# Kernel tuning notes

Hardware: AMD Instinct MI355X
Metric: run time of the kernel (lower is better)

The kernel has to match this reference:

```python
import jax, jax.numpy as jnp
import numpy as np

DIM = 1024
H = 16
HD = DIM // H
SCALE = HD ** -0.5
LAMBDA_INIT = 0.1
EPS = 1e-6


def setup_inputs() -> dict:
    key0 = jax.random.key(0)
    ks = jax.random.split(key0, 12)
    B, Nq, Nk = 2, 1024, 2048
    w = 0.02
    inp = {
        "query": jax.random.normal(ks[0], (B, Nq, DIM), jnp.float32),
        "key": jax.random.normal(ks[1], (B, Nk, DIM), jnp.float32),
        "value": jax.random.normal(ks[2], (B, Nk, DIM), jnp.float32),
        "qpos": jax.random.randint(ks[3], (B, Nq), 0, Nq, jnp.int32),
        "kpos": jax.random.randint(ks[4], (B, Nk), 0, Nk, jnp.int32),
        "q1_w": jax.random.normal(ks[5], (DIM, DIM), jnp.float32) * w,
        "q2_w": jax.random.normal(ks[6], (DIM, DIM), jnp.float32) * w,
        "kv1_w": jax.random.normal(ks[7], (2 * DIM, DIM), jnp.float32) * w,
        "kv2_w": jax.random.normal(ks[8], (2 * DIM, DIM), jnp.float32) * w,
        "proj_w": jax.random.normal(ks[9], (DIM, DIM), jnp.float32) * w,
        "proj_b": jnp.zeros((DIM,), jnp.float32),
        "norm_w": jnp.ones((DIM,), jnp.float32),
        "lambda_1": jnp.ones((1, H, 1, 1), jnp.float32),
        # layer_idx=0, max_layer=12 -> scale = 1/12
        "lambda_2": jnp.full((1, H, 1, 1), 1.0 - LAMBDA_INIT * (1.0 / 12.0), jnp.float32),
    }
    return inp


def _split_heads(x, B, N):
    # [B, N, DIM] -> [B, H, N, HD]
    return x.reshape(B, N, H, HD).transpose(0, 2, 1, 3)


def reference(query, key, value, qpos, kpos, q1_w, q2_w, kv1_w, kv2_w,
              proj_w, proj_b, norm_w, lambda_1, lambda_2):
    B, Nq, C = query.shape
    Nk = key.shape[1]

    q1 = _split_heads(query @ q1_w.T, B, Nq)
    q2 = _split_heads(query @ q2_w.T, B, Nq)

    kv1 = (key @ kv1_w.T).reshape(B, Nk, 2, H, HD).transpose(2, 0, 3, 1, 4)
    k1, v1 = kv1[0], kv1[1]  # [B, H, Nk, HD]
    kv2 = (key @ kv2_w.T).reshape(B, Nk, 2, H, HD).transpose(2, 0, 3, 1, 4)
    k2 = kv2[0]

    attn1 = jax.nn.softmax(jnp.einsum('bhqd,bhkd->bhqk', q1, k1) * SCALE, axis=-1)
    attn2 = jax.nn.softmax(jnp.einsum('bhqd,bhkd->bhqk', q2, k2) * SCALE, axis=-1)

    lambda_full = lambda_1 - lambda_2 + LAMBDA_INIT  # [1, H, 1, 1]
    diff_attn = attn1 - lambda_full * attn2

    x = jnp.einsum('bhqk,bhkd->bhqd', diff_attn, v1)
    x = x.transpose(0, 2, 1, 3).reshape(B, Nq, C)

    # RMSNorm (computed in float32 like the original)
    xf = x.astype(jnp.float32)
    xf = xf * jax.lax.rsqrt(jnp.mean(xf * xf, axis=-1, keepdims=True) + EPS) * norm_w
    x = xf.astype(x.dtype)

    return x @ proj_w.T + proj_b
```

## Files before the change

### kernel.cpp

```cpp
#include <hip/hip_runtime.h>
#include <cstdint>

typedef unsigned short u16;
typedef __bf16 bf16x8 __attribute__((ext_vector_type(8)));
typedef float f32x4 __attribute__((ext_vector_type(4)));
typedef float f32x16 __attribute__((ext_vector_type(16)));
typedef uint32_t u32x4 __attribute__((ext_vector_type(4)));

#define SCALE_LOG2E (0.125f * 1.44269504088896340736f)

__device__ __forceinline__ u16 f2bf(float f) {
    uint32_t u = __builtin_bit_cast(uint32_t, f);
    u += 0x7fff + ((u >> 16) & 1);
    return (u16)(u >> 16);
}
__device__ __forceinline__ float bf2f(u16 u) {
    return __builtin_bit_cast(float, (uint32_t)u << 16);
}

__device__ __forceinline__ void gload_lds16(const void* g, void* l) {
    __builtin_amdgcn_global_load_lds(
        (__attribute__((address_space(1))) void*)g,
        (__attribute__((address_space(3))) void*)l, 16, 0, 0);
}

__global__ __launch_bounds__(256) void cvt_all(const float* __restrict__ s0,
                                               const float* __restrict__ s1,
                                               const float* __restrict__ s2,
                                               const float* __restrict__ s3,
                                               const float* __restrict__ s4,
                                               const float* __restrict__ s5,
                                               const float* __restrict__ s6,
                                               u16* __restrict__ d0, u16* __restrict__ d1,
                                               u16* __restrict__ d2, u16* __restrict__ d3,
                                               u16* __restrict__ d4) {
    int i = blockIdx.x * 256 + threadIdx.x;
    const float* src;
    u16* dst;
    int off;
    if (i < 524288)       { src = s0; dst = d0; off = i; }
    else if (i < 1572864) { src = s1; dst = d1; off = i - 524288; }
    else if (i < 1835008) { src = s2; dst = d2; off = i - 1572864; }
    else if (i < 2097152) { src = s3; dst = d2 + (size_t)1024 * 1024; off = i - 1835008; }
    else if (i < 2621440) { src = s4; dst = d3; off = i - 2097152; }
    else if (i < 2883584) { src = s5; dst = d3 + (size_t)2048 * 1024; off = i - 2621440; }
    else                  { src = s6; dst = d4; off = i - 2883584; }
    float4 v = ((const float4*)src)[off];
    ushort4 o;
    o.x = f2bf(v.x); o.y = f2bf(v.y); o.z = f2bf(v.z); o.w = f2bf(v.w);
    ((ushort4*)dst)[off] = o;
}

__global__ __launch_bounds__(256) void gemm_qkv(const u16* __restrict__ Wq,
                                                const u16* __restrict__ Xq,
                                                const u16* __restrict__ Wkv,
                                                const u16* __restrict__ Xk,
                                                u16* __restrict__ q1s, u16* __restrict__ q2s,
                                                u16* __restrict__ k1f, u16* __restrict__ v1f,
                                                u16* __restrict__ k2f) {
    __shared__ u16 As[2][128 * 32];
    __shared__ u16 Bs[2][128 * 32];
    const int K = 1024;
    const int bid = blockIdx.x;
    int mode, bm, bn;
    const u16 *A, *B;
    if (bid < 256) {
        mode = 0; bm = bid >> 4; bn = bid & 15; A = Wq; B = Xq;
    } else {
        int t = bid - 256;
        mode = 1; bm = t % 24; bn = t / 24; A = Wkv; B = Xk;
    }
    const int tid = threadIdx.x;
    const int l = tid & 63, w = tid >> 6;
    const int c = l & 15, g = l >> 4;
    const int wr = w >> 1, wc = w & 1;

    f32x4 acc[4][4];
#pragma unroll
    for (int i = 0; i < 4; i++)
#pragma unroll
        for (int j = 0; j < 4; j++) acc[i][j] = f32x4{0.f, 0.f, 0.f, 0.f};

    const u16* Abase = A + (size_t)(bm * 128) * K;
    const u16* Bbase = B + (size_t)(bn * 128) * K;
    const int r0 = 32 * w + (l >> 2);
    const int chsw = ((l & 3) ^ ((l >> 3) & 3)) * 8;

    const int gsw = 8 * (g ^ ((c >> 1) & 3));

    int cur = 0;
    gload_lds16(Abase + (size_t)r0 * K + chsw,        &As[0][32 * w * 32]);
    gload_lds16(Abase + (size_t)(r0 + 16) * K + chsw, &As[0][(32 * w + 16) * 32]);
    gload_lds16(Bbase + (size_t)r0 * K + chsw,        &Bs[0][32 * w * 32]);
    gload_lds16(Bbase + (size_t)(r0 + 16) * K + chsw, &Bs[0][(32 * w + 16) * 32]);
    __syncthreads();

    for (int t = 0; t < 32; ++t) {
        if (t < 31) {
            const int kb = (t + 1) * 32;
            gload_lds16(Abase + (size_t)r0 * K + kb + chsw,        &As[cur ^ 1][32 * w * 32]);
            gload_lds16(Abase + (size_t)(r0 + 16) * K + kb + chsw, &As[cur ^ 1][(32 * w + 16) * 32]);
            gload_lds16(Bbase + (size_t)r0 * K + kb + chsw,        &Bs[cur ^ 1][32 * w * 32]);
            gload_lds16(Bbase + (size_t)(r0 + 16) * K + kb + chsw, &Bs[cur ^ 1][(32 * w + 16) * 32]);
        }
        bf16x8 af[4], bfr[4];
#pragma unroll
        for (int mi = 0; mi < 4; mi++)
            af[mi] = *(const bf16x8*)&As[cur][(64 * wr + 16 * mi + c) * 32 + gsw];
#pragma unroll
        for (int ni = 0; ni < 4; ni++)
            bfr[ni] = *(const bf16x8*)&Bs[cur][(64 * wc + 16 * ni + c) * 32 + gsw];
#pragma unroll
        for (int mi = 0; mi < 4; mi++)
#pragma unroll
            for (int ni = 0; ni < 4; ni++)
                acc[mi][ni] = __builtin_amdgcn_mfma_f32_16x16x32_bf16(
                    af[mi], bfr[ni], acc[mi][ni], 0, 0, 0);
        __syncthreads();
        cur ^= 1;
    }

#pragma unroll
    for (int mi = 0; mi < 4; mi++) {
        const int m0 = bm * 128 + 64 * wr + 16 * mi + 4 * g;
#pragma unroll
        for (int ni = 0; ni < 4; ni++) {
            const int n = bn * 128 + 64 * wc + 16 * ni + c;
            f32x4 v = acc[mi][ni];
            if (mode == 0) {
                int half = m0 >> 10, feat = m0 & 1023;
                int h = feat >> 6, hd0 = feat & 63;
                int b = n >> 10, nq = n & 1023;
                int bh = b * 16 + h;
                u16* dst = half ? q2s : q1s;
                size_t idx = ((size_t)(bh * 32 + (nq >> 5)) * 4 + (hd0 >> 4)) * 512
                           + (((hd0 >> 3) & 1) * 32 + (nq & 31)) * 8 + (hd0 & 7);
                ushort4 o;
                o.x = f2bf(v[0] * SCALE_LOG2E); o.y = f2bf(v[1] * SCALE_LOG2E);
                o.z = f2bf(v[2] * SCALE_LOG2E); o.w = f2bf(v[3] * SCALE_LOG2E);
                *(ushort4*)(dst + idx) = o;
            } else {
                int b = n >> 11, nk = n & 2047;
                if (m0 < 1024) {
                    int h = m0 >> 6, hd0 = m0 & 63, bh = b * 16 + h;
                    size_t idx = ((size_t)(bh * 64 + (nk >> 5)) * 4 + (hd0 >> 4)) * 512
                               + (((hd0 >> 3) & 1) * 32 + (nk & 31)) * 8 + (hd0 & 7);
                    ushort4 o;
                    o.x = f2bf(v[0]); o.y = f2bf(v[1]); o.z = f2bf(v[2]); o.w = f2bf(v[3]);
                    *(ushort4*)(k1f + idx) = o;
                } else if (m0 < 2048) {
                    int feat = m0 - 1024, h = feat >> 6, hd0 = feat & 63, bh = b * 16 + h;
#pragma unroll
                    for (int j = 0; j < 4; j++) {
                        int hd = hd0 + j;
                        size_t idx = ((size_t)(bh * 128 + (nk >> 4)) * 2 + (hd >> 5)) * 512
                                   + (((nk >> 3) & 1) * 32 + (hd & 31)) * 8 + (nk & 7);
                        v1f[idx] = f2bf(v[j]);
                    }
                } else {
                    int feat = m0 - 2048, h = feat >> 6, hd0 = feat & 63, bh = b * 16 + h;
                    size_t idx = ((size_t)(bh * 64 + (nk >> 5)) * 4 + (hd0 >> 4)) * 512
                               + (((hd0 >> 3) & 1) * 32 + (nk & 31)) * 8 + (hd0 & 7);
                    ushort4 o;
                    o.x = f2bf(v[0]); o.y = f2bf(v[1]); o.z = f2bf(v[2]); o.w = f2bf(v[3]);
                    *(ushort4*)(k2f + idx) = o;
                }
            }
        }
    }
}

__global__ __launch_bounds__(256) void gemm_proj(const u16* __restrict__ A,
                                                 const u16* __restrict__ B,
                                                 float* __restrict__ fo,
                                                 const float* __restrict__ bias) {
    __shared__ u16 As[2][128 * 32];
    __shared__ u16 Bs[2][64 * 32];
    const int K = 1024;
    const int bm = blockIdx.x >> 4, bn = blockIdx.x & 15;
    const int tid = threadIdx.x;
    const int l = tid & 63, w = tid >> 6;
    const int c = l & 15, g = l >> 4;
    const int wr = w >> 1, wc = w & 1;

    f32x4 acc[4][2];
#pragma unroll
    for (int i = 0; i < 4; i++)
#pragma unroll
        for (int j = 0; j < 2; j++) acc[i][j] = f32x4{0.f, 0.f, 0.f, 0.f};

    const u16* Abase = A + (size_t)(bm * 128) * K;
    const u16* Bbase = B + (size_t)(bn * 64) * K;
    const int rA = 32 * w + (l >> 2);
    const int rB = 16 * w + (l >> 2);
    const int chsw = ((l & 3) ^ ((l >> 3) & 3)) * 8;
    const int gsw = 8 * (g ^ ((c >> 1) & 3));

    int cur = 0;
    gload_lds16(Abase + (size_t)rA * K + chsw,        &As[0][32 * w * 32]);
    gload_lds16(Abase + (size_t)(rA + 16) * K + chsw, &As[0][(32 * w + 16) * 32]);
    gload_lds16(Bbase + (size_t)rB * K + chsw,        &Bs[0][16 * w * 32]);
    __syncthreads();

    for (int t = 0; t < 32; ++t) {
        if (t < 31) {
            const int kb = (t + 1) * 32;
            gload_lds16(Abase + (size_t)rA * K + kb + chsw,        &As[cur ^ 1][32 * w * 32]);
            gload_lds16(Abase + (size_t)(rA + 16) * K + kb + chsw, &As[cur ^ 1][(32 * w + 16) * 32]);
            gload_lds16(Bbase + (size_t)rB * K + kb + chsw,        &Bs[cur ^ 1][16 * w * 32]);
        }
        bf16x8 af[4], bfr[2];
#pragma unroll
        for (int mi = 0; mi < 4; mi++)
            af[mi] = *(const bf16x8*)&As[cur][(64 * wr + 16 * mi + c) * 32 + gsw];
#pragma unroll
        for (int ni = 0; ni < 2; ni++)
            bfr[ni] = *(const bf16x8*)&Bs[cur][(32 * wc + 16 * ni + c) * 32 + gsw];
#pragma unroll
        for (int mi = 0; mi < 4; mi++)
#pragma unroll
            for (int ni = 0; ni < 2; ni++)
                acc[mi][ni] = __builtin_amdgcn_mfma_f32_16x16x32_bf16(
                    af[mi], bfr[ni], acc[mi][ni], 0, 0, 0);
        __syncthreads();
        cur ^= 1;
    }

#pragma unroll
    for (int mi = 0; mi < 4; mi++)
#pragma unroll
        for (int ni = 0; ni < 2; ni++)
#pragma unroll
            for (int j = 0; j < 4; j++) {
                int m = bm * 128 + 64 * wr + 16 * mi + 4 * g + j;
                int n = bn * 64 + 32 * wc + 16 * ni + c;
                fo[(size_t)m * 1024 + n] = acc[mi][ni][j] + bias[n];
            }
}

__global__ __launch_bounds__(256) void attn_kernel(const u16* __restrict__ q1s,
                                                   const u16* __restrict__ q2s,
                                                   const u16* __restrict__ k1fm,
                                                   const u16* __restrict__ k2fm,
                                                   const u16* __restrict__ v1fm,
                                                   u16* __restrict__ Opart,
                                                   float* __restrict__ Lpart) {
    const int tid = threadIdx.x;
    const int l = tid & 63, w = tid >> 6;
    const int c5 = l & 31, hf = l >> 5;
    const int bid = blockIdx.x;
    const int xcd = bid & 7, slot = bid >> 3;
    const int bh = xcd * 4 + (slot >> 5);
    const int r = slot & 31;
    const int qt = r >> 2, s = r & 3;
    const int b = bh >> 4, head = bh & 15;
    const int q0 = qt * 128 + w * 32;

    bf16x8 qB1[4], qB2[4];
    {
        const u16* p1 = q1s + ((size_t)(bh * 32 + (q0 >> 5)) * 4) * 512 + l * 8;
        const u16* p2 = q2s + ((size_t)(bh * 32 + (q0 >> 5)) * 4) * 512 + l * 8;
#pragma unroll
        for (int d = 0; d < 4; d++) {
            qB1[d] = *(const bf16x8*)(p1 + d * 512);
            qB2[d] = *(const bf16x8*)(p2 + d * 512);
        }
    }

    f32x16 O1[2], O2[2];
#pragma unroll
    for (int dh = 0; dh < 2; dh++)
#pragma unroll
        for (int i = 0; i < 16; i++) { O1[dh][i] = 0.f; O2[dh][i] = 0.f; }
    float la1 = 0.f, la2 = 0.f;

    const u16* k1t = k1fm + (size_t)bh * 64 * 2048;
    const u16* k2t = k2fm + (size_t)bh * 64 * 2048;
    const u16* vt  = v1fm + (size_t)bh * 128 * 1024;

    for (int it = 0; it < 16; it++) {
        const int t32 = s * 16 + it;
        const u16* p1 = k1t + (size_t)t32 * 2048 + l * 8;
        const u16* p2 = k2t + (size_t)t32 * 2048 + l * 8;
        const u16* pv = vt + (size_t)t32 * 2048 + l * 8;

        bf16x8 kA1[4], kA2[4];
#pragma unroll
        for (int d = 0; d < 4; d++) {
            kA1[d] = *(const bf16x8*)(p1 + d * 512);
            kA2[d] = *(const bf16x8*)(p2 + d * 512);
        }
        bf16x8 vB[2][2];
#pragma unroll
        for (int kk = 0; kk < 2; kk++)
#pragma unroll
            for (int dh = 0; dh < 2; dh++)
                vB[dh][kk] = *(const bf16x8*)(pv + (2 * kk + dh) * 512);

        {
            f32x16 S;
#pragma unroll
            for (int i = 0; i < 16; i++) S[i] = 0.f;
#pragma unroll
            for (int d = 0; d < 4; d++)
                S = __builtin_amdgcn_mfma_f32_32x32x16_bf16(kA1[d], qB1[d], S, 0, 0, 0);
            uint32_t dpk[8];
#pragma unroll
            for (int i = 0; i < 8; i++) {
                float pa = __builtin_exp2f(S[2 * i]);
                float pb = __builtin_exp2f(S[2 * i + 1]);
                la1 += pa + pb;
                asm("v_cvt_pk_bf16_f32 %0, %1, %2" : "=v"(dpk[i]) : "v"(pa), "v"(pb));
            }
            uint32_t a0 = dpk[0], b0 = dpk[2], a1 = dpk[1], b1 = dpk[3];
            asm("v_permlane32_swap_b32 %0, %1" : "+v"(a0), "+v"(b0));
            asm("v_permlane32_swap_b32 %0, %1" : "+v"(a1), "+v"(b1));
            u32x4 t0 = {a0, a1, b0, b1};
            bf16x8 pf0 = __builtin_bit_cast(bf16x8, t0);
            uint32_t a2 = dpk[4], b2 = dpk[6], a3 = dpk[5], b3 = dpk[7];
            asm("v_permlane32_swap_b32 %0, %1" : "+v"(a2), "+v"(b2));
            asm("v_permlane32_swap_b32 %0, %1" : "+v"(a3), "+v"(b3));
            u32x4 t1 = {a2, a3, b2, b3};
            bf16x8 pf1 = __builtin_bit_cast(bf16x8, t1);
#pragma unroll
            for (int dh = 0; dh < 2; dh++) {
                O1[dh] = __builtin_amdgcn_mfma_f32_32x32x16_bf16(pf0, vB[dh][0], O1[dh], 0, 0, 0);
                O1[dh] = __builtin_amdgcn_mfma_f32_32x32x16_bf16(pf1, vB[dh][1], O1[dh], 0, 0, 0);
            }
        }
        {
            f32x16 S;
#pragma unroll
            for (int i = 0; i < 16; i++) S[i] = 0.f;
#pragma unroll
            for (int d = 0; d < 4; d++)
                S = __builtin_amdgcn_mfma_f32_32x32x16_bf16(kA2[d], qB2[d], S, 0, 0, 0);
            uint32_t dpk[8];
#pragma unroll
            for (int i = 0; i < 8; i++) {
                float pa = __builtin_exp2f(S[2 * i]);
                float pb = __builtin_exp2f(S[2 * i + 1]);
                la2 += pa + pb;
                asm("v_cvt_pk_bf16_f32 %0, %1, %2" : "=v"(dpk[i]) : "v"(pa), "v"(pb));
            }
            uint32_t a0 = dpk[0], b0 = dpk[2], a1 = dpk[1], b1 = dpk[3];
            asm("v_permlane32_swap_b32 %0, %1" : "+v"(a0), "+v"(b0));
            asm("v_permlane32_swap_b32 %0, %1" : "+v"(a1), "+v"(b1));
            u32x4 t0 = {a0, a1, b0, b1};
            bf16x8 pf0 = __builtin_bit_cast(bf16x8, t0);
            uint32_t a2 = dpk[4], b2 = dpk[6], a3 = dpk[5], b3 = dpk[7];
            asm("v_permlane32_swap_b32 %0, %1" : "+v"(a2), "+v"(b2));
            asm("v_permlane32_swap_b32 %0, %1" : "+v"(a3), "+v"(b3));
            u32x4 t1 = {a2, a3, b2, b3};
            bf16x8 pf1 = __builtin_bit_cast(bf16x8, t1);
#pragma unroll
            for (int dh = 0; dh < 2; dh++) {
                O2[dh] = __builtin_amdgcn_mfma_f32_32x32x16_bf16(pf0, vB[dh][0], O2[dh], 0, 0, 0);
                O2[dh] = __builtin_amdgcn_mfma_f32_32x32x16_bf16(pf1, vB[dh][1], O2[dh], 0, 0, 0);
            }
        }
    }

    la1 += __shfl_xor(la1, 32, 64);
    la2 += __shfl_xor(la2, 32, 64);

#pragma unroll
    for (int dh = 0; dh < 2; dh++)
#pragma unroll
        for (int rr = 0; rr < 16; rr++) {
            int qrow = (rr & 3) + 8 * (rr >> 2) + 4 * hf;
            size_t rowg = (size_t)b * 1024 + q0 + qrow;
            size_t col = head * 64 + dh * 32 + c5;
            Opart[((size_t)(s * 2 + 0) * 2048 + rowg) * 1024 + col] = f2bf(O1[dh][rr]);
            Opart[((size_t)(s * 2 + 1) * 2048 + rowg) * 1024 + col] = f2bf(O2[dh][rr]);
        }
    if (hf == 0) {
        size_t rowg = (size_t)b * 1024 + q0 + c5;
        Lpart[((size_t)(s * 2 + 0) * 2048 + rowg) * 16 + head] = la1;
        Lpart[((size_t)(s * 2 + 1) * 2048 + rowg) * 16 + head] = la2;
    }
}

__global__ __launch_bounds__(256) void combine_rms(const u16* __restrict__ Opart,
                                                   const float* __restrict__ Lpart,
                                                   const float* __restrict__ lam1,
                                                   const float* __restrict__ lam2,
                                                   const float* __restrict__ nw,
                                                   u16* __restrict__ xn) {
    const int row = blockIdx.x, t = threadIdx.x;
    const int h = t >> 4;
    float a1[4] = {0.f, 0.f, 0.f, 0.f}, a2[4] = {0.f, 0.f, 0.f, 0.f};
    float li1 = 0.f, li2 = 0.f;
#pragma unroll
    for (int s = 0; s < 4; s++) {
        ushort4 u1 = ((const ushort4*)(Opart + ((size_t)(s * 2 + 0) * 2048 + row) * 1024))[t];
        ushort4 u2 = ((const ushort4*)(Opart + ((size_t)(s * 2 + 1) * 2048 + row) * 1024))[t];
        a1[0] += bf2f(u1.x); a1[1] += bf2f(u1.y); a1[2] += bf2f(u1.z); a1[3] += bf2f(u1.w);
        a2[0] += bf2f(u2.x); a2[1] += bf2f(u2.y); a2[2] += bf2f(u2.z); a2[3] += bf2f(u2.w);
        li1 += Lpart[((size_t)(s * 2 + 0) * 2048 + row) * 16 + h];
        li2 += Lpart[((size_t)(s * 2 + 1) * 2048 + row) * 16 + h];
    }
    float lam = lam1[h] - lam2[h] + 0.1f;
    float i1 = 1.0f / li1, i2 = lam / li2;
    float x0 = a1[0] * i1 - a2[0] * i2;
    float x1 = a1[1] * i1 - a2[1] * i2;
    float x2 = a1[2] * i1 - a2[2] * i2;
    float x3 = a1[3] * i1 - a2[3] * i2;
    float ss = x0 * x0 + x1 * x1 + x2 * x2 + x3 * x3;
#pragma unroll
    for (int off = 1; off < 64; off <<= 1) ss += __shfl_xor(ss, off, 64);
    __shared__ float ws4[4];
    if ((t & 63) == 0) ws4[t >> 6] = ss;
    __syncthreads();
    float tot = ws4[0] + ws4[1] + ws4[2] + ws4[3];
    float rs = rsqrtf(tot * (1.0f / 1024.0f) + 1e-6f);
    float4 wv = ((const float4*)nw)[t];
    ushort4 o;
    o.x = f2bf(x0 * rs * wv.x);
    o.y = f2bf(x1 * rs * wv.y);
    o.z = f2bf(x2 * rs * wv.z);
    o.w = f2bf(x3 * rs * wv.w);
    ((ushort4*)(xn + (size_t)row * 1024))[t] = o;
}

extern "C" void kernel_launch(void* const* d_in, const int* in_sizes, int n_in,
                              void* d_out, int out_size, void* d_ws, size_t ws_size,
                              hipStream_t stream) {
    const float* query  = (const float*)d_in[0];
    const float* key    = (const float*)d_in[1];
    const float* q1_w   = (const float*)d_in[5];
    const float* q2_w   = (const float*)d_in[6];
    const float* kv1_w  = (const float*)d_in[7];
    const float* kv2_w  = (const float*)d_in[8];
    const float* proj_w = (const float*)d_in[9];
    const float* proj_b = (const float*)d_in[10];
    const float* norm_w = (const float*)d_in[11];
    const float* lam1   = (const float*)d_in[12];
    const float* lam2   = (const float*)d_in[13];
    float* out = (float*)d_out;

    char* ws = (char*)d_ws;
    size_t off = 0;
    auto alloc = [&](size_t bytes) {
        void* p = ws + off;
        off += (bytes + 255) & ~(size_t)255;
        return p;
    };
    u16* Xq   = (u16*)alloc((size_t)2048 * 1024 * 2);
    u16* Xk   = (u16*)alloc((size_t)4096 * 1024 * 2);
    u16* Wq   = (u16*)alloc((size_t)2048 * 1024 * 2);
    u16* Wkv  = (u16*)alloc((size_t)3072 * 1024 * 2);
    u16* Wp   = (u16*)alloc((size_t)1024 * 1024 * 2);
    u16* q1sb = (u16*)alloc((size_t)32 * 1024 * 64 * 2);
    u16* q2sb = (u16*)alloc((size_t)32 * 1024 * 64 * 2);
    u16* k1fb = (u16*)alloc((size_t)32 * 2048 * 64 * 2);
    u16* k2fb = (u16*)alloc((size_t)32 * 2048 * 64 * 2);
    u16* v1fb = (u16*)alloc((size_t)32 * 64 * 2048 * 2);
    u16* Opart = (u16*)alloc((size_t)8 * 2048 * 1024 * 2);
    float* Lpart = (float*)alloc((size_t)8 * 2048 * 16 * 4);
    u16* xn   = (u16*)alloc((size_t)2048 * 1024 * 2);

    cvt_all<<<12288, 256, 0, stream>>>(query, key, q1_w, q2_w, kv1_w, kv2_w, proj_w,
                                       Xq, Xk, Wq, Wkv, Wp);

    gemm_qkv<<<1024, 256, 0, stream>>>(Wq, Xq, Wkv, Xk, q1sb, q2sb, k1fb, v1fb, k2fb);

    attn_kernel<<<1024, 256, 0, stream>>>(q1sb, q2sb, k1fb, k2fb, v1fb, Opart, Lpart);

    combine_rms<<<2048, 256, 0, stream>>>(Opart, Lpart, lam1, lam2, norm_w, xn);

    gemm_proj<<<256, 256, 0, stream>>>(xn, Wp, out, proj_b);
}
```

Before: 260.4 us.

## Stage shared K1/K2/V tiles through double-buffered LDS in attention kernel

```diff
diff --git a/kernel.cpp b/kernel.cpp
--- a/kernel.cpp
+++ b/kernel.cpp
@@ -85,7 +85,6 @@
     const u16* Bbase = B + (size_t)(bn * 128) * K;
     const int r0 = 32 * w + (l >> 2);
     const int chsw = ((l & 3) ^ ((l >> 3) & 3)) * 8;
-
     const int gsw = 8 * (g ^ ((c >> 1) & 3));
 
     int cur = 0;
@@ -245,6 +244,7 @@
                                                    const u16* __restrict__ v1fm,
                                                    u16* __restrict__ Opart,
                                                    float* __restrict__ Lpart) {
+    __shared__ u16 kv[2][6144];
     const int tid = threadIdx.x;
     const int l = tid & 63, w = tid >> 6;
     const int c5 = l & 31, hf = l >> 5;
@@ -256,6 +256,20 @@
     const int b = bh >> 4, head = bh & 15;
     const int q0 = qt * 128 + w * 32;
 
+    const u16* k1t = k1fm + (size_t)bh * 64 * 2048;
+    const u16* k2t = k2fm + (size_t)bh * 64 * 2048;
+    const u16* vt  = v1fm + (size_t)bh * 128 * 1024;
+    const u16* bases[3] = {k1t, k2t, vt};
+
+    auto stage = [&](int buf, int t32) {
+#pragma unroll
+        for (int j = 0; j < 3; j++) {
+            int q = w * 3 + j;
+            const u16* src = bases[q >> 2] + (size_t)t32 * 2048 + (q & 3) * 512 + l * 8;
+            gload_lds16(src, &kv[buf][q * 512]);
+        }
+    };
+
     bf16x8 qB1[4], qB2[4];
     {
         const u16* p1 = q1s + ((size_t)(bh * 32 + (q0 >> 5)) * 4) * 512 + l * 8;
@@ -274,36 +288,25 @@
         for (int i = 0; i < 16; i++) { O1[dh][i] = 0.f; O2[dh][i] = 0.f; }
     float la1 = 0.f, la2 = 0.f;
 
-    const u16* k1t = k1fm + (size_t)bh * 64 * 2048;
-    const u16* k2t = k2fm + (size_t)bh * 64 * 2048;
-    const u16* vt  = v1fm + (size_t)bh * 128 * 1024;
+    stage(0, s * 16);
+    __syncthreads();
+    int cur = 0;
 
     for (int it = 0; it < 16; it++) {
-        const int t32 = s * 16 + it;
-        const u16* p1 = k1t + (size_t)t32 * 2048 + l * 8;
-        const u16* p2 = k2t + (size_t)t32 * 2048 + l * 8;
-        const u16* pv = vt + (size_t)t32 * 2048 + l * 8;
-
-        bf16x8 kA1[4], kA2[4];
-#pragma unroll
-        for (int d = 0; d < 4; d++) {
-            kA1[d] = *(const bf16x8*)(p1 + d * 512);
-            kA2[d] = *(const bf16x8*)(p2 + d * 512);
-        }
-        bf16x8 vB[2][2];
-#pragma unroll
-        for (int kk = 0; kk < 2; kk++)
-#pragma unroll
-            for (int dh = 0; dh < 2; dh++)
-                vB[dh][kk] = *(const bf16x8*)(pv + (2 * kk + dh) * 512);
-
+        if (it < 15) stage(cur ^ 1, s * 16 + it + 1);
+
+        const u16* bufp = &kv[cur][0];
         {
+            bf16x8 kA[4];
+#pragma unroll
+            for (int d = 0; d < 4; d++)
+                kA[d] = *(const bf16x8*)(bufp + d * 512 + l * 8);
             f32x16 S;
 #pragma unroll
             for (int i = 0; i < 16; i++) S[i] = 0.f;
 #pragma unroll
             for (int d = 0; d < 4; d++)
-                S = __builtin_amdgcn_mfma_f32_32x32x16_bf16(kA1[d], qB1[d], S, 0, 0, 0);
+                S = __builtin_amdgcn_mfma_f32_32x32x16_bf16(kA[d], qB1[d], S, 0, 0, 0);
             uint32_t dpk[8];
 #pragma unroll
             for (int i = 0; i < 8; i++) {
@@ -324,17 +327,23 @@
             bf16x8 pf1 = __builtin_bit_cast(bf16x8, t1);
 #pragma unroll
             for (int dh = 0; dh < 2; dh++) {
-                O1[dh] = __builtin_amdgcn_mfma_f32_32x32x16_bf16(pf0, vB[dh][0], O1[dh], 0, 0, 0);
-                O1[dh] = __builtin_amdgcn_mfma_f32_32x32x16_bf16(pf1, vB[dh][1], O1[dh], 0, 0, 0);
+                bf16x8 v0 = *(const bf16x8*)(bufp + 4096 + dh * 512 + l * 8);
+                bf16x8 v1 = *(const bf16x8*)(bufp + 4096 + (2 + dh) * 512 + l * 8);
+                O1[dh] = __builtin_amdgcn_mfma_f32_32x32x16_bf16(pf0, v0, O1[dh], 0, 0, 0);
+                O1[dh] = __builtin_amdgcn_mfma_f32_32x32x16_bf16(pf1, v1, O1[dh], 0, 0, 0);
             }
         }
         {
+            bf16x8 kA[4];
+#pragma unroll
+            for (int d = 0; d < 4; d++)
+                kA[d] = *(const bf16x8*)(bufp + 2048 + d * 512 + l * 8);
             f32x16 S;
 #pragma unroll
             for (int i = 0; i < 16; i++) S[i] = 0.f;
 #pragma unroll
             for (int d = 0; d < 4; d++)
-                S = __builtin_amdgcn_mfma_f32_32x32x16_bf16(kA2[d], qB2[d], S, 0, 0, 0);
+                S = __builtin_amdgcn_mfma_f32_32x32x16_bf16(kA[d], qB2[d], S, 0, 0, 0);
             uint32_t dpk[8];
 #pragma unroll
             for (int i = 0; i < 8; i++) {
@@ -355,10 +364,14 @@
             bf16x8 pf1 = __builtin_bit_cast(bf16x8, t1);
 #pragma unroll
             for (int dh = 0; dh < 2; dh++) {
-                O2[dh] = __builtin_amdgcn_mfma_f32_32x32x16_bf16(pf0, vB[dh][0], O2[dh], 0, 0, 0);
-                O2[dh] = __builtin_amdgcn_mfma_f32_32x32x16_bf16(pf1, vB[dh][1], O2[dh], 0, 0, 0);
-            }
-        }
+                bf16x8 v0 = *(const bf16x8*)(bufp + 4096 + dh * 512 + l * 8);
+                bf16x8 v1 = *(const bf16x8*)(bufp + 4096 + (2 + dh) * 512 + l * 8);
+                O2[dh] = __builtin_amdgcn_mfma_f32_32x32x16_bf16(pf0, v0, O2[dh], 0, 0, 0);
+                O2[dh] = __builtin_amdgcn_mfma_f32_32x32x16_bf16(pf1, v1, O2[dh], 0, 0, 0);
+            }
+        }
+        __syncthreads();
+        cur ^= 1;
     }
 
     la1 += __shfl_xor(la1, 32, 64);
```

Result: no change. 262.8 us (+0.9%).
